# Performance work log

Hardware: AMD Instinct MI355X
Metric: run time of the kernel (lower is better)

Reference implementation:

```python
import jax, jax.numpy as jnp
import numpy as np

B, H, S, DK = 2, 16, 2048, 64

def setup_inputs() -> dict:
    key = jax.random.key(0)
    kq, kk, kv, km = jax.random.split(key, 4)
    queries = jax.random.normal(kq, (B, H, S, DK), dtype=jnp.float32)
    keys = jax.random.normal(kk, (B, H, S, DK), dtype=jnp.float32)
    values = jax.random.normal(kv, (B, H, S, DK), dtype=jnp.float32)
    mask = jax.random.randint(km, (B, S, S), 0, 2, dtype=jnp.int32)
    return {"queries": queries, "keys": keys, "values": values, "mask": mask}

def reference(queries, keys, values, mask):
    d_k = queries.shape[-1]
    scale = 1.0 / np.sqrt(d_k).astype(np.float32)
    # [B,H,S,S]
    scores = jnp.einsum('bhqd,bhkd->bhqk', queries, keys) * scale
    m = mask[:, None, :, :]  # broadcast over heads, like mask.unsqueeze(1)
    scores = jnp.where(m == 0, jnp.asarray(-1e9, scores.dtype), scores)
    attn = jax.nn.softmax(scores, axis=-1)
    return jnp.einsum('bhqk,bhkd->bhqd', attn, values)
```

## Files before the change

kernel.cpp:

```cpp
#include <hip/hip_runtime.h>


#define S_   2048
#define D_   64
#define H_   16
#define B_   2
#define BH_  32
#define KVB  64
#define NKV  (S_/KVB)
#define QPB  128
#define NQT  (S_/QPB)
#define NQS  2

typedef __attribute__((ext_vector_type(8))) _Float16 f16x8;
typedef __attribute__((ext_vector_type(4))) _Float16 f16x4;
typedef __attribute__((ext_vector_type(4))) float    f32x4;

static __device__ __forceinline__ void async16(const void* g, void* l) {
  __builtin_amdgcn_global_load_lds(
      (const __attribute__((address_space(1))) void*)g,
      (__attribute__((address_space(3))) void*)l, 16, 0, 0);
}

__global__ __launch_bounds__(256) void cvt_f32_f16_k(
    const float* __restrict__ src, _Float16* __restrict__ dst, int n4) {
  int i = blockIdx.x * blockDim.x + threadIdx.x;
  int st = gridDim.x * blockDim.x;
  for (; i < n4; i += st) {
    float4 v = ((const float4*)src)[i];
    f16x4 o = {(_Float16)v.x, (_Float16)v.y, (_Float16)v.z, (_Float16)v.w};
    *(f16x4*)(dst + 4 * (size_t)i) = o;
  }
}

__global__ __launch_bounds__(256) void transpose_v_k(
    const float* __restrict__ V, _Float16* __restrict__ Vt) {
  __shared__ float tile[64][65];
  int bid = blockIdx.x;
  int st = bid & 31;
  int bh = bid >> 5;
  const float* src = V + ((size_t)bh * S_ + st * 64) * D_;
  int r = threadIdx.x >> 2, cq = threadIdx.x & 3;
#pragma unroll
  for (int j = 0; j < 4; ++j) {
    float4 v = ((const float4*)(src + (size_t)r * D_))[cq + 4 * j];
    int col = (cq + 4 * j) * 4;
    tile[r][col + 0] = v.x; tile[r][col + 1] = v.y;
    tile[r][col + 2] = v.z; tile[r][col + 3] = v.w;
  }
  __syncthreads();
  int d = threadIdx.x >> 2, s = (threadIdx.x & 3) * 16;
  _Float16 tmp[16];
#pragma unroll
  for (int j = 0; j < 16; ++j) tmp[j] = (_Float16)tile[s + j][d];
  _Float16* dstp = Vt + ((size_t)bh * D_ + d) * S_ + st * 64 + s;
  *(f16x8*)(dstp)     = *((f16x8*)tmp);
  *(f16x8*)(dstp + 8) = *((f16x8*)tmp + 1);
}

__global__ __launch_bounds__(256) void pack_mask_k(
    const int* __restrict__ mask, unsigned long long* __restrict__ bits, int nwords) {
  int lane = threadIdx.x & 63;
  int w0 = (blockIdx.x * blockDim.x + threadIdx.x) >> 6;
  int nw = (gridDim.x * blockDim.x) >> 6;
  for (int w = w0; w < nwords; w += nw) {
    int m = mask[(size_t)w * 64 + lane];
    unsigned long long bal = __ballot(m != 0);
    if (lane == 0) bits[w] = bal;
  }
}

__global__ __launch_bounds__(256) void attn_fwd(
    const _Float16* __restrict__ Qh, const _Float16* __restrict__ Kh,
    const _Float16* __restrict__ Vth, const unsigned long long* __restrict__ Mb,
    float* __restrict__ Out) {
  __shared__ _Float16 Kt[KVB * D_];
  __shared__ _Float16 Vt[D_ * KVB];
  __shared__ _Float16 Pl[4 * NQS][16 * KVB];

  const int tid = threadIdx.x;
  const int lane = tid & 63;
  const int wid = tid >> 6;
  const int g = lane >> 4;
  const int c = lane & 15;
  const int c7 = c & 7;

  int bid = blockIdx.x;
  bid = (bid & 7) * 64 + (bid >> 3);
  const int qt = bid & (NQT - 1);
  const int bh = bid >> 4;
  const int b = bh >> 4;

  const int q0 = qt * QPB + wid * (NQS * 16);

  const _Float16* Kbh = Kh + (size_t)bh * S_ * D_;
  const _Float16* Vbh = Vth + (size_t)bh * D_ * S_;

  f16x8 qf[NQS][2];
#pragma unroll
  for (int qs = 0; qs < NQS; ++qs) {
    const _Float16* qp = Qh + ((size_t)bh * S_ + q0 + qs * 16 + c) * D_ + g * 8;
    qf[qs][0] = *(const f16x8*)(qp);
    qf[qs][1] = *(const f16x8*)(qp + 32);
  }

  f32x4 accO[NQS][4];
#pragma unroll
  for (int qs = 0; qs < NQS; ++qs)
#pragma unroll
    for (int dp = 0; dp < 4; ++dp) accO[qs][dp] = {0.f, 0.f, 0.f, 0.f};

  float m_run[NQS], l_run[NQS];
#pragma unroll
  for (int qs = 0; qs < NQS; ++qs) { m_run[qs] = -INFINITY; l_run[qs] = 0.f; }

  for (int kv = 0; kv < NKV; ++kv) {
    __syncthreads();
#pragma unroll
    for (int it = 0; it < 2; ++it) {
      int idx = it * 256 + tid;
      int row = idx >> 3, gr = idx & 7;
      async16(Kbh + ((size_t)(kv * KVB + row)) * D_ + ((gr ^ (row & 7)) << 3),
              &Kt[(idx & ~63) * 8]);
      async16(Vbh + (size_t)row * S_ + kv * KVB + ((gr ^ (row & 7)) << 3),
              &Vt[(idx & ~63) * 8]);
    }
    __syncthreads();

    f16x8 kfr[4][2];
#pragma unroll
    for (int kt = 0; kt < 4; ++kt)
#pragma unroll
      for (int dc = 0; dc < 2; ++dc) {
        int row = kt * 16 + c;
        kfr[kt][dc] = *(const f16x8*)(&Kt[row * D_ + (((dc * 4 + g) ^ c7) << 3)]);
      }

    f32x4 st[NQS][4];
#pragma unroll
    for (int qs = 0; qs < NQS; ++qs)
#pragma unroll
      for (int kt = 0; kt < 4; ++kt) {
        f32x4 a = {0.f, 0.f, 0.f, 0.f};
        a = __builtin_amdgcn_mfma_f32_16x16x32_f16(kfr[kt][0], qf[qs][0], a, 0, 0, 0);
        a = __builtin_amdgcn_mfma_f32_16x16x32_f16(kfr[kt][1], qf[qs][1], a, 0, 0, 0);
        st[qs][kt] = a;
      }

#pragma unroll
    for (int qs = 0; qs < NQS; ++qs) {
      unsigned long long mw = Mb[((size_t)b * S_ + q0 + qs * 16 + c) * NKV + kv];
      float s[16];
      float mx = -INFINITY;
#pragma unroll
      for (int kt = 0; kt < 4; ++kt)
#pragma unroll
        for (int r = 0; r < 4; ++r) {
          float v = st[qs][kt][r] * 0.125f;
          int kl = kt * 16 + 4 * g + r;
          v = ((mw >> kl) & 1ull) ? v : -1.0e9f;
          s[kt * 4 + r] = v;
          mx = fmaxf(mx, v);
        }
      mx = fmaxf(mx, __shfl_xor(mx, 16));
      mx = fmaxf(mx, __shfl_xor(mx, 32));
      float mn = fmaxf(m_run[qs], mx);
      float rs = 0.f;
      f16x4 ph[4];
#pragma unroll
      for (int kt = 0; kt < 4; ++kt)
#pragma unroll
        for (int r = 0; r < 4; ++r) {
          float pe = __expf(s[kt * 4 + r] - mn);
          rs += pe;
          ph[kt][r] = (_Float16)pe;
        }
      rs += __shfl_xor(rs, 16);
      rs += __shfl_xor(rs, 32);
      float cf = __expf(m_run[qs] - mn);
      m_run[qs] = mn;
      l_run[qs] = l_run[qs] * cf + rs;
#pragma unroll
      for (int dp = 0; dp < 4; ++dp) accO[qs][dp] = accO[qs][dp] * cf;
      _Float16* pw = Pl[wid * NQS + qs] + c * KVB;
#pragma unroll
      for (int kt = 0; kt < 4; ++kt) {
        int gp = (2 * kt + (g >> 1)) ^ c7;
        *(f16x4*)(pw + gp * 8 + (g & 1) * 4) = ph[kt];
      }
    }
    asm volatile("s_waitcnt lgkmcnt(0)" ::: "memory");
    __builtin_amdgcn_sched_barrier(0);

#pragma unroll
    for (int ks = 0; ks < 2; ++ks) {
      f16x8 vfr[4];
#pragma unroll
      for (int dp = 0; dp < 4; ++dp) {
        int row = dp * 16 + c;
        vfr[dp] = *(const f16x8*)(&Vt[row * KVB + (((4 * ks + g) ^ c7) << 3)]);
      }
#pragma unroll
      for (int qs = 0; qs < NQS; ++qs) {
        const _Float16* pr = Pl[wid * NQS + qs] + c * KVB + (((4 * ks + g) ^ c7) << 3);
        f16x8 pf = *(const f16x8*)pr;
#pragma unroll
        for (int dp = 0; dp < 4; ++dp)
          accO[qs][dp] = __builtin_amdgcn_mfma_f32_16x16x32_f16(vfr[dp], pf, accO[qs][dp], 0, 0, 0);
      }
    }
  }

#pragma unroll
  for (int qs = 0; qs < NQS; ++qs) {
    float inv = 1.0f / l_run[qs];
    float* op = Out + ((size_t)bh * S_ + q0 + qs * 16 + c) * D_;
#pragma unroll
    for (int dp = 0; dp < 4; ++dp) {
      f32x4 o = accO[qs][dp] * inv;
      *(f32x4*)(op + dp * 16 + 4 * g) = o;
    }
  }
}

extern "C" void kernel_launch(void* const* d_in, const int* in_sizes, int n_in,
                              void* d_out, int out_size, void* d_ws, size_t ws_size,
                              hipStream_t stream) {
  const float* Q = (const float*)d_in[0];
  const float* K = (const float*)d_in[1];
  const float* V = (const float*)d_in[2];
  const int*   M = (const int*)d_in[3];
  float* Out = (float*)d_out;

  const size_t NE = (size_t)B_ * H_ * S_ * D_;
  _Float16* Qh  = (_Float16*)d_ws;
  _Float16* Kh  = Qh + NE;
  _Float16* Vth = Kh + NE;
  unsigned long long* Mb = (unsigned long long*)(Vth + NE);

  cvt_f32_f16_k<<<1024, 256, 0, stream>>>(Q, Qh, (int)(NE / 4));
  cvt_f32_f16_k<<<1024, 256, 0, stream>>>(K, Kh, (int)(NE / 4));
  transpose_v_k<<<1024, 256, 0, stream>>>(V, Vth);
  pack_mask_k<<<1024, 256, 0, stream>>>(M, Mb, B_ * S_ * (S_ / 64));
  attn_fwd<<<NQT * BH_, 256, 0, stream>>>(Qh, Kh, Vth, Mb, Out);
}
```

Baseline: 217.5 us.

## Fuse prepass kernels, fold scale into K, use exp2 with lazy rescale and mask LUT

Merges the K conversion, V transpose and mask packing into one launch, and drops the separate Q conversion by loading fp32 Q directly in the attention kernel. K is prescaled by log2(e)/sqrt(d) so the softmax can use exp2. The running-max rescale now runs only when the max grows by more than a threshold. Masking becomes an fp16 multiply by a LUT-derived 0/1 pair, and the row sum uses dot2. Blocks are restructured to 512 threads with one 16-row Q slice per wave, and fp16 packing uses round-toward-zero conversion, which changes numerics slightly and relies on the lazy-rescale bound to stay in range.

```diff
diff --git a/kernel.cpp b/kernel.cpp
--- a/kernel.cpp
+++ b/kernel.cpp
@@ -10,10 +10,12 @@
 #define NKV  (S_/KVB)
 #define QPB  128
 #define NQT  (S_/QPB)
-#define NQS  2
+
+#define KSCALE 0.18033688f
 
 typedef __attribute__((ext_vector_type(8))) _Float16 f16x8;
 typedef __attribute__((ext_vector_type(4))) _Float16 f16x4;
+typedef __attribute__((ext_vector_type(2))) _Float16 f16x2;
 typedef __attribute__((ext_vector_type(4))) float    f32x4;
 
 static __device__ __forceinline__ void async16(const void* g, void* l) {
@@ -22,61 +24,68 @@
       (__attribute__((address_space(3))) void*)l, 16, 0, 0);
 }
 
-__global__ __launch_bounds__(256) void cvt_f32_f16_k(
-    const float* __restrict__ src, _Float16* __restrict__ dst, int n4) {
-  int i = blockIdx.x * blockDim.x + threadIdx.x;
-  int st = gridDim.x * blockDim.x;
-  for (; i < n4; i += st) {
-    float4 v = ((const float4*)src)[i];
-    f16x4 o = {(_Float16)v.x, (_Float16)v.y, (_Float16)v.z, (_Float16)v.w};
-    *(f16x4*)(dst + 4 * (size_t)i) = o;
-  }
-}
-
-__global__ __launch_bounds__(256) void transpose_v_k(
-    const float* __restrict__ V, _Float16* __restrict__ Vt) {
+static __device__ __forceinline__ f16x2 pkrtz(float a, float b) {
+  return __builtin_bit_cast(f16x2, __builtin_amdgcn_cvt_pkrtz(a, b));
+}
+
+__global__ __launch_bounds__(256) void prepass_k(
+    const float* __restrict__ K, const float* __restrict__ V,
+    const int* __restrict__ M,
+    _Float16* __restrict__ Kh, _Float16* __restrict__ Vth,
+    unsigned long long* __restrict__ Mb) {
   __shared__ float tile[64][65];
-  int bid = blockIdx.x;
-  int st = bid & 31;
-  int bh = bid >> 5;
-  const float* src = V + ((size_t)bh * S_ + st * 64) * D_;
-  int r = threadIdx.x >> 2, cq = threadIdx.x & 3;
-#pragma unroll
-  for (int j = 0; j < 4; ++j) {
-    float4 v = ((const float4*)(src + (size_t)r * D_))[cq + 4 * j];
-    int col = (cq + 4 * j) * 4;
-    tile[r][col + 0] = v.x; tile[r][col + 1] = v.y;
-    tile[r][col + 2] = v.z; tile[r][col + 3] = v.w;
-  }
-  __syncthreads();
-  int d = threadIdx.x >> 2, s = (threadIdx.x & 3) * 16;
-  _Float16 tmp[16];
-#pragma unroll
-  for (int j = 0; j < 16; ++j) tmp[j] = (_Float16)tile[s + j][d];
-  _Float16* dstp = Vt + ((size_t)bh * D_ + d) * S_ + st * 64 + s;
-  *(f16x8*)(dstp)     = *((f16x8*)tmp);
-  *(f16x8*)(dstp + 8) = *((f16x8*)tmp + 1);
-}
-
-__global__ __launch_bounds__(256) void pack_mask_k(
-    const int* __restrict__ mask, unsigned long long* __restrict__ bits, int nwords) {
-  int lane = threadIdx.x & 63;
-  int w0 = (blockIdx.x * blockDim.x + threadIdx.x) >> 6;
-  int nw = (gridDim.x * blockDim.x) >> 6;
-  for (int w = w0; w < nwords; w += nw) {
-    int m = mask[(size_t)w * 64 + lane];
-    unsigned long long bal = __ballot(m != 0);
-    if (lane == 0) bits[w] = bal;
-  }
-}
-
-__global__ __launch_bounds__(256) void attn_fwd(
-    const _Float16* __restrict__ Qh, const _Float16* __restrict__ Kh,
+  const int bidx = blockIdx.x;
+  const int tid = threadIdx.x;
+  if (bidx < 1024) {
+    int st = bidx & 31;
+    int bh = bidx >> 5;
+    const float* src = V + ((size_t)bh * S_ + st * 64) * D_;
+    int r = tid >> 2, cq = tid & 3;
+#pragma unroll
+    for (int j = 0; j < 4; ++j) {
+      float4 v = ((const float4*)(src + (size_t)r * D_))[cq + 4 * j];
+      int col = (cq + 4 * j) * 4;
+      tile[r][col + 0] = v.x; tile[r][col + 1] = v.y;
+      tile[r][col + 2] = v.z; tile[r][col + 3] = v.w;
+    }
+    __syncthreads();
+    int d = tid >> 2, s = (tid & 3) * 16;
+    _Float16 tmp[16];
+#pragma unroll
+    for (int j = 0; j < 16; ++j) tmp[j] = (_Float16)tile[s + j][d];
+    _Float16* dstp = Vth + ((size_t)bh * D_ + d) * S_ + st * 64 + s;
+    *(f16x8*)(dstp)     = *((f16x8*)tmp);
+    *(f16x8*)(dstp + 8) = *((f16x8*)tmp + 1);
+  } else if (bidx < 1536) {
+    int idx = (bidx - 1024) * 256 + tid;
+#pragma unroll
+    for (int j = 0; j < 8; ++j) {
+      int i = idx + j * 131072;
+      float4 v = ((const float4*)K)[i];
+      f16x4 o = {(_Float16)(v.x * KSCALE), (_Float16)(v.y * KSCALE),
+                 (_Float16)(v.z * KSCALE), (_Float16)(v.w * KSCALE)};
+      *(f16x4*)(Kh + 4 * (size_t)i) = o;
+    }
+  } else {
+    int lane = tid & 63;
+    int wb = (bidx - 1536) * 256 + (tid >> 6) * 64;
+    for (int i = 0; i < 64; ++i) {
+      int w = wb + i;
+      int m = M[(size_t)w * 64 + lane];
+      unsigned long long bal = __ballot(m != 0);
+      if (lane == 0) Mb[w] = bal;
+    }
+  }
+}
+
+__global__ __launch_bounds__(512, 4) void attn_fwd(
+    const float* __restrict__ Qf, const _Float16* __restrict__ Kh,
     const _Float16* __restrict__ Vth, const unsigned long long* __restrict__ Mb,
     float* __restrict__ Out) {
   __shared__ _Float16 Kt[KVB * D_];
   __shared__ _Float16 Vt[D_ * KVB];
-  __shared__ _Float16 Pl[4 * NQS][16 * KVB];
+  __shared__ _Float16 Pl[8][16 * KVB];
+  __shared__ unsigned long long MLUT[16];
 
   const int tid = threadIdx.x;
   const int lane = tid & 63;
@@ -85,141 +94,135 @@
   const int c = lane & 15;
   const int c7 = c & 7;
 
+  if (tid < 16) {
+    unsigned w0 = ((tid & 1) ? 0x3C00u : 0u) | ((tid & 2) ? 0x3C000000u : 0u);
+    unsigned w1 = ((tid & 4) ? 0x3C00u : 0u) | ((tid & 8) ? 0x3C000000u : 0u);
+    MLUT[tid] = (unsigned long long)w0 | ((unsigned long long)w1 << 32);
+  }
+
   int bid = blockIdx.x;
   bid = (bid & 7) * 64 + (bid >> 3);
   const int qt = bid & (NQT - 1);
   const int bh = bid >> 4;
   const int b = bh >> 4;
 
-  const int q0 = qt * QPB + wid * (NQS * 16);
-
-  const _Float16* Kbh = Kh + (size_t)bh * S_ * D_;
-  const _Float16* Vbh = Vth + (size_t)bh * D_ * S_;
-
-  f16x8 qf[NQS][2];
-#pragma unroll
-  for (int qs = 0; qs < NQS; ++qs) {
-    const _Float16* qp = Qh + ((size_t)bh * S_ + q0 + qs * 16 + c) * D_ + g * 8;
-    qf[qs][0] = *(const f16x8*)(qp);
-    qf[qs][1] = *(const f16x8*)(qp + 32);
-  }
-
-  f32x4 accO[NQS][4];
-#pragma unroll
-  for (int qs = 0; qs < NQS; ++qs)
-#pragma unroll
-    for (int dp = 0; dp < 4; ++dp) accO[qs][dp] = {0.f, 0.f, 0.f, 0.f};
-
-  float m_run[NQS], l_run[NQS];
-#pragma unroll
-  for (int qs = 0; qs < NQS; ++qs) { m_run[qs] = -INFINITY; l_run[qs] = 0.f; }
+  const int q0 = qt * QPB + wid * 16;
+
+  f16x8 qf[2];
+  {
+    const float* qp = Qf + ((size_t)bh * S_ + q0 + c) * D_ + 8 * g;
+    _Float16 t[16];
+#pragma unroll
+    for (int j = 0; j < 8; ++j) t[j] = (_Float16)qp[j];
+#pragma unroll
+    for (int j = 0; j < 8; ++j) t[8 + j] = (_Float16)qp[32 + j];
+    qf[0] = *(f16x8*)t;
+    qf[1] = *((f16x8*)t + 1);
+  }
+
+  f32x4 accO[4];
+#pragma unroll
+  for (int dp = 0; dp < 4; ++dp) accO[dp] = {0.f, 0.f, 0.f, 0.f};
+  float m_run = -INFINITY, l_run = 0.f;
+
+  const int srow = tid >> 3, sgr = tid & 7;
+  const _Float16* kp = Kh + (size_t)bh * S_ * D_ + (size_t)srow * D_ + ((sgr ^ (srow & 7)) << 3);
+  const _Float16* vp = Vth + (size_t)bh * D_ * S_ + (size_t)srow * S_ + ((sgr ^ (srow & 7)) << 3);
+  _Float16* ldk = &Kt[(tid & ~63) * 8];
+  _Float16* ldv = &Vt[(tid & ~63) * 8];
+  const unsigned long long* pmb = Mb + ((size_t)b * S_ + q0 + c) * NKV;
+
+  const f16x2 one2 = {(_Float16)1.0f, (_Float16)1.0f};
 
   for (int kv = 0; kv < NKV; ++kv) {
     __syncthreads();
-#pragma unroll
-    for (int it = 0; it < 2; ++it) {
-      int idx = it * 256 + tid;
-      int row = idx >> 3, gr = idx & 7;
-      async16(Kbh + ((size_t)(kv * KVB + row)) * D_ + ((gr ^ (row & 7)) << 3),
-              &Kt[(idx & ~63) * 8]);
-      async16(Vbh + (size_t)row * S_ + kv * KVB + ((gr ^ (row & 7)) << 3),
-              &Vt[(idx & ~63) * 8]);
-    }
+    async16(kp, ldk);
+    async16(vp, ldv);
+    kp += KVB * D_;
+    vp += KVB;
+    unsigned long long mw = pmb[kv];
     __syncthreads();
 
-    f16x8 kfr[4][2];
+    f32x4 st[4];
+#pragma unroll
+    for (int kt = 0; kt < 4; ++kt) {
+      int row = kt * 16 + c;
+      f16x8 k0 = *(const f16x8*)(&Kt[row * D_ + (((0 * 4 + g) ^ c7) << 3)]);
+      f16x8 k1 = *(const f16x8*)(&Kt[row * D_ + (((1 * 4 + g) ^ c7) << 3)]);
+      f32x4 a = {0.f, 0.f, 0.f, 0.f};
+      a = __builtin_amdgcn_mfma_f32_16x16x32_f16(k0, qf[0], a, 0, 0, 0);
+      a = __builtin_amdgcn_mfma_f32_16x16x32_f16(k1, qf[1], a, 0, 0, 0);
+      st[kt] = a;
+    }
+
+    float pmax = st[0][0];
 #pragma unroll
     for (int kt = 0; kt < 4; ++kt)
 #pragma unroll
-      for (int dc = 0; dc < 2; ++dc) {
-        int row = kt * 16 + c;
-        kfr[kt][dc] = *(const f16x8*)(&Kt[row * D_ + (((dc * 4 + g) ^ c7) << 3)]);
-      }
-
-    f32x4 st[NQS][4];
-#pragma unroll
-    for (int qs = 0; qs < NQS; ++qs)
-#pragma unroll
-      for (int kt = 0; kt < 4; ++kt) {
-        f32x4 a = {0.f, 0.f, 0.f, 0.f};
-        a = __builtin_amdgcn_mfma_f32_16x16x32_f16(kfr[kt][0], qf[qs][0], a, 0, 0, 0);
-        a = __builtin_amdgcn_mfma_f32_16x16x32_f16(kfr[kt][1], qf[qs][1], a, 0, 0, 0);
-        st[qs][kt] = a;
-      }
-
-#pragma unroll
-    for (int qs = 0; qs < NQS; ++qs) {
-      unsigned long long mw = Mb[((size_t)b * S_ + q0 + qs * 16 + c) * NKV + kv];
-      float s[16];
-      float mx = -INFINITY;
-#pragma unroll
-      for (int kt = 0; kt < 4; ++kt)
-#pragma unroll
-        for (int r = 0; r < 4; ++r) {
-          float v = st[qs][kt][r] * 0.125f;
-          int kl = kt * 16 + 4 * g + r;
-          v = ((mw >> kl) & 1ull) ? v : -1.0e9f;
-          s[kt * 4 + r] = v;
-          mx = fmaxf(mx, v);
-        }
-      mx = fmaxf(mx, __shfl_xor(mx, 16));
-      mx = fmaxf(mx, __shfl_xor(mx, 32));
-      float mn = fmaxf(m_run[qs], mx);
-      float rs = 0.f;
-      f16x4 ph[4];
-#pragma unroll
-      for (int kt = 0; kt < 4; ++kt)
-#pragma unroll
-        for (int r = 0; r < 4; ++r) {
-          float pe = __expf(s[kt * 4 + r] - mn);
-          rs += pe;
-          ph[kt][r] = (_Float16)pe;
-        }
-      rs += __shfl_xor(rs, 16);
-      rs += __shfl_xor(rs, 32);
-      float cf = __expf(m_run[qs] - mn);
-      m_run[qs] = mn;
-      l_run[qs] = l_run[qs] * cf + rs;
-#pragma unroll
-      for (int dp = 0; dp < 4; ++dp) accO[qs][dp] = accO[qs][dp] * cf;
-      _Float16* pw = Pl[wid * NQS + qs] + c * KVB;
-#pragma unroll
-      for (int kt = 0; kt < 4; ++kt) {
-        int gp = (2 * kt + (g >> 1)) ^ c7;
-        *(f16x4*)(pw + gp * 8 + (g & 1) * 4) = ph[kt];
-      }
+      for (int r = 0; r < 4; ++r) pmax = fmaxf(pmax, st[kt][r]);
+    pmax = fmaxf(pmax, __shfl_xor(pmax, 16));
+    pmax = fmaxf(pmax, __shfl_xor(pmax, 32));
+    if (!__all(pmax - m_run <= 8.f)) {
+      float mn = fmaxf(m_run, pmax);
+      float cf = __builtin_amdgcn_exp2f(m_run - mn);
+      l_run *= cf;
+#pragma unroll
+      for (int dp = 0; dp < 4; ++dp) accO[dp] = accO[dp] * cf;
+      m_run = mn;
+    }
+
+    const unsigned mlo = (unsigned)mw, mhi = (unsigned)(mw >> 32);
+    float rs = 0.f;
+    f16x2 wv[8];
+#pragma unroll
+    for (int kt = 0; kt < 4; ++kt) {
+      unsigned nib = (((kt < 2) ? mlo : mhi) >> (((kt & 1) << 4) + 4 * g)) & 0xFu;
+      unsigned long long lut = MLUT[nib];
+      f16x2 m01 = __builtin_bit_cast(f16x2, (unsigned)lut);
+      f16x2 m23 = __builtin_bit_cast(f16x2, (unsigned)(lut >> 32));
+      f16x2 p01 = pkrtz(__builtin_amdgcn_exp2f(st[kt][0] - m_run),
+                        __builtin_amdgcn_exp2f(st[kt][1] - m_run));
+      f16x2 p23 = pkrtz(__builtin_amdgcn_exp2f(st[kt][2] - m_run),
+                        __builtin_amdgcn_exp2f(st[kt][3] - m_run));
+      wv[2 * kt]     = p01 * m01;
+      wv[2 * kt + 1] = p23 * m23;
+      rs = __builtin_amdgcn_fdot2(wv[2 * kt], one2, rs, false);
+      rs = __builtin_amdgcn_fdot2(wv[2 * kt + 1], one2, rs, false);
+    }
+    rs += __shfl_xor(rs, 16);
+    rs += __shfl_xor(rs, 32);
+    l_run += rs;
+
+    _Float16* pw = Pl[wid] + c * KVB;
+#pragma unroll
+    for (int kt = 0; kt < 4; ++kt) {
+      int gp = (2 * kt + (g >> 1)) ^ c7;
+      uint2 wpair = {__builtin_bit_cast(unsigned, wv[2 * kt]),
+                     __builtin_bit_cast(unsigned, wv[2 * kt + 1])};
+      *(uint2*)(pw + gp * 8 + (g & 1) * 4) = wpair;
     }
     asm volatile("s_waitcnt lgkmcnt(0)" ::: "memory");
     __builtin_amdgcn_sched_barrier(0);
 
 #pragma unroll
     for (int ks = 0; ks < 2; ++ks) {
-      f16x8 vfr[4];
+      const _Float16* pr = Pl[wid] + c * KVB + (((4 * ks + g) ^ c7) << 3);
+      f16x8 pf = *(const f16x8*)pr;
 #pragma unroll
       for (int dp = 0; dp < 4; ++dp) {
         int row = dp * 16 + c;
-        vfr[dp] = *(const f16x8*)(&Vt[row * KVB + (((4 * ks + g) ^ c7) << 3)]);
+        f16x8 vfr = *(const f16x8*)(&Vt[row * KVB + (((4 * ks + g) ^ c7) << 3)]);
+        accO[dp] = __builtin_amdgcn_mfma_f32_16x16x32_f16(vfr, pf, accO[dp], 0, 0, 0);
       }
-#pragma unroll
-      for (int qs = 0; qs < NQS; ++qs) {
-        const _Float16* pr = Pl[wid * NQS + qs] + c * KVB + (((4 * ks + g) ^ c7) << 3);
-        f16x8 pf = *(const f16x8*)pr;
-#pragma unroll
-        for (int dp = 0; dp < 4; ++dp)
-          accO[qs][dp] = __builtin_amdgcn_mfma_f32_16x16x32_f16(vfr[dp], pf, accO[qs][dp], 0, 0, 0);
-      }
-    }
-  }
-
-#pragma unroll
-  for (int qs = 0; qs < NQS; ++qs) {
-    float inv = 1.0f / l_run[qs];
-    float* op = Out + ((size_t)bh * S_ + q0 + qs * 16 + c) * D_;
-#pragma unroll
-    for (int dp = 0; dp < 4; ++dp) {
-      f32x4 o = accO[qs][dp] * inv;
-      *(f32x4*)(op + dp * 16 + 4 * g) = o;
-    }
+    }
+  }
+
+  float inv = 1.0f / l_run;
+  float* op = Out + ((size_t)bh * S_ + q0 + c) * D_;
+#pragma unroll
+  for (int dp = 0; dp < 4; ++dp) {
+    f32x4 o = accO[dp] * inv;
+    *(f32x4*)(op + dp * 16 + 4 * g) = o;
   }
 }
 
@@ -233,14 +236,10 @@
   float* Out = (float*)d_out;
 
   const size_t NE = (size_t)B_ * H_ * S_ * D_;
-  _Float16* Qh  = (_Float16*)d_ws;
-  _Float16* Kh  = Qh + NE;
+  _Float16* Kh  = (_Float16*)d_ws;
   _Float16* Vth = Kh + NE;
   unsigned long long* Mb = (unsigned long long*)(Vth + NE);
 
-  cvt_f32_f16_k<<<1024, 256, 0, stream>>>(Q, Qh, (int)(NE / 4));
-  cvt_f32_f16_k<<<1024, 256, 0, stream>>>(K, Kh, (int)(NE / 4));
-  transpose_v_k<<<1024, 256, 0, stream>>>(V, Vth);
-  pack_mask_k<<<1024, 256, 0, stream>>>(M, Mb, B_ * S_ * (S_ / 64));
-  attn_fwd<<<NQT * BH_, 256, 0, stream>>>(Qh, Kh, Vth, Mb, Out);
-}
+  prepass_k<<<2048, 256, 0, stream>>>(K, V, M, Kh, Vth, Mb);
+  attn_fwd<<<NQT * BH_, 512, 0, stream>>>(Q, Kh, Vth, Mb, Out);
+}
```

After: 201.6 us. -7.3%, faster.
